# Kernel tuning notes

Hardware: AMD Instinct MI355X
Metric: run time of the kernel (lower is better)

## Reference

```python
import jax, jax.numpy as jnp
import numpy as np

B, N, F_IN = 32, 1024, 64   # batch, num_nodes, diffusion_size[0]
K = 3                        # expansion_step
H = 2                        # num_heads
HID, RAW, OUT, CLS = 128, 128, 128, 2
D1, D2 = 128, 128            # diffusion_size[1], diffusion_size[2]
CAT = D1 + RAW               # concat dim fed to attention (h || h_prime) = 256


def setup_inputs() -> dict:
    key = jax.random.key(0)
    ks = jax.random.split(key, 40)
    g = lambda i, shape: jax.random.normal(ks[i], shape, dtype=jnp.float32) * 0.05
    inp = {
        'X': jax.random.normal(ks[0], (B, N, F_IN), dtype=jnp.float32),
        'A': jax.random.uniform(ks[1], (B, N, N), dtype=jnp.float32),
        # transition tensors / mixing weights (only the 2 layers used in forward)
        'T': g(2, (2, K, N, N)),
        'theta': jnp.full((2, K), 1.0 / K, dtype=jnp.float32),
        # raw feature projection
        'W_raw': g(3, (F_IN, RAW)), 'b_raw': jnp.zeros((RAW,), jnp.float32),
        # diffusion layer linears
        'Wd0': g(4, (F_IN, D1)), 'bd0': jnp.zeros((D1,), jnp.float32),
        'Wd1': g(5, (D1, D2)),   'bd1': jnp.zeros((D2,), jnp.float32),
        # final classifier
        'W_fin': g(6, (OUT, CLS)), 'b_fin': jnp.zeros((CLS,), jnp.float32),
    }
    # two CatMultiAttn blocks: q/k/v projections (CAT->HID), out proj (HID->OUT)
    i = 7
    for l in range(2):
        for nm in ('q', 'k', 'v'):
            inp[f'W{nm}{l}'] = g(i, (CAT, HID)); i += 1
            inp[f'b{nm}{l}'] = jnp.zeros((HID,), jnp.float32)
        inp[f'Wo{l}'] = g(i, (HID, OUT)); i += 1
        inp[f'bo{l}'] = jnp.zeros((OUT,), jnp.float32)
    return inp


def _diffusion(theta_l, T_l, h, A, W, b):
    # Q = sum_k theta_k * T_k  (generalized graph diffusion transition)
    Q = jnp.einsum('k,kij->ij', theta_l, T_l)          # [N,N]
    S = Q[None, :, :] * A                               # [B,N,N] mask by adjacency
    z = jnp.einsum('bij,bjf->bif', S, h)                # diffuse features
    return jax.nn.relu(z @ W + b)


def _cat_attn(h, hp, Wq, bq, Wk, bk, Wv, bv, Wo, bo):
    # concatenate diffused + embedding features, multi-head self-attn over nodes
    x = jnp.concatenate([h, hp], axis=-1)               # [B,N,CAT]
    b, n, _ = x.shape
    q = (x @ Wq + bq).reshape(b, n, H, HID // H)
    k = (x @ Wk + bk).reshape(b, n, H, HID // H)
    v = (x @ Wv + bv).reshape(b, n, H, HID // H)
    scale = jnp.asarray(1.0 / np.sqrt(HID // H), x.dtype)
    s = jnp.einsum('bnhd,bmhd->bhnm', q, k) * scale     # [B,H,N,N]
    p = jax.nn.softmax(s, axis=-1)
    ctx = jnp.einsum('bhnm,bmhd->bnhd', p, v).reshape(b, n, HID)
    return jax.nn.relu(ctx @ Wo + bo)


def reference(X, A, T, theta, W_raw, b_raw, Wd0, bd0, Wd1, bd1,
              W_fin, b_fin,
              Wq0, bq0, Wk0, bk0, Wv0, bv0, Wo0, bo0,
              Wq1, bq1, Wk1, bk1, Wv1, bv1, Wo1, bo1):
    theta_soft = jax.nn.softmax(theta, axis=-1)         # [2,K]
    h_prime = X @ W_raw + b_raw                          # [B,N,RAW]
    # layer 0
    h = _diffusion(theta_soft[0], T[0], X, A, Wd0, bd0)  # [B,N,D1]
    h_prime = _cat_attn(h, h_prime, Wq0, bq0, Wk0, bk0, Wv0, bv0, Wo0, bo0)
    # layer 1 (residual fusion)
    h = _diffusion(theta_soft[1], T[1], h, A, Wd1, bd1)  # [B,N,D2]
    h_prime = h_prime + _cat_attn(h, h_prime, Wq1, bq1, Wk1, bk1, Wv1, bv1, Wo1, bo1)
    return h_prime @ W_fin + b_fin                       # [B,N,CLS]
```

## Files before the change

kernel.cpp:

```cpp
#include <hip/hip_runtime.h>
#include <hip/hip_bf16.h>

typedef __hip_bfloat16 bf16;
typedef __attribute__((ext_vector_type(8))) short s8b;
typedef __attribute__((ext_vector_type(4))) short s4b;
typedef __attribute__((ext_vector_type(4))) float f4;

#define BB   32
#define NN   1024
#define FIN  64
#define HEADS 2
#define DH   64
#define HIDD 128
#define SZQ  ((size_t)BB * NN * HIDD)

__device__ __forceinline__ ushort f2bf(float x) {
    bf16 h = __float2bfloat16(x);
    return *(ushort*)&h;
}
__device__ __forceinline__ float bfbits2f(ushort h) {
    union { uint u; float f; } c; c.u = (uint)h << 16; return c.f;
}
__device__ __forceinline__ uint pk_bf16(float lo, float hi) {
    return (uint)f2bf(lo) | ((uint)f2bf(hi) << 16);
}
union U8 { short s[8]; s8b v; };
union U4 { short s[4]; s4b v; };
union UQ { ushort u[8]; s8b v; };

__global__ __launch_bounds__(256) void setup_kernel(
        const float* __restrict__ raw, const float* __restrict__ d0,
        const float* __restrict__ d1,
        const float* __restrict__ q0w, const float* __restrict__ k0w,
        const float* __restrict__ v0w, const float* __restrict__ o0w,
        const float* __restrict__ q1w, const float* __restrict__ k1w,
        const float* __restrict__ v1w, const float* __restrict__ o1w,
        ushort* __restrict__ Whi, ushort* __restrict__ Wlo,
        const float* __restrict__ T, const float* __restrict__ theta,
        ushort* __restrict__ Q0hi, ushort* __restrict__ Q0lo,
        ushort* __restrict__ Q1hi, ushort* __restrict__ Q1lo,
        const float* __restrict__ X,
        ushort* __restrict__ XT_hi, ushort* __restrict__ XT_lo) {
    __shared__ float tile[64][65];
    const int bid = blockIdx.x;
    const int t = threadIdx.x;
    if (bid < 1024) {
        int id = bid * 256 + t;
        const float* src; int K, off;
        if      (id <   8192) { src = raw; K =  64; off = 0; }
        else if (id <  16384) { src = d0;  K =  64; off = 8192; }
        else if (id <  32768) { src = d1;  K = 128; off = 16384; }
        else if (id <  65536) { src = q0w; K = 256; off = 32768; }
        else if (id <  98304) { src = k0w; K = 256; off = 65536; }
        else if (id < 131072) { src = v0w; K = 256; off = 98304; }
        else if (id < 147456) { src = o0w; K = 128; off = 131072; }
        else if (id < 180224) { src = q1w; K = 256; off = 147456; }
        else if (id < 212992) { src = k1w; K = 256; off = 180224; }
        else if (id < 245760) { src = v1w; K = 256; off = 212992; }
        else                  { src = o1w; K = 128; off = 245760; }
        int il = id - off;
        int k = il >> 7, c = il & 127;
        float w = src[il];
        ushort h = f2bf(w);
        Whi[off + c * K + k] = h;
        Wlo[off + c * K + k] = f2bf(w - bfbits2f(h));
    } else if (bid < 1536) {
        const int tb = bid - 1024;
        const int b  = tb >> 4;
        const int n0 = (tb & 15) * 64;
        {
            int nl = t >> 2, f0 = (t & 3) * 16;
            const float* xp = X + ((size_t)b * NN + n0 + nl) * 64 + f0;
#pragma unroll
            for (int i = 0; i < 16; i += 4)
                *(float4*)&tile[nl][f0 + i] = *(const float4*)(xp + i);
        }
        __syncthreads();
        {
            int f = t >> 2, n1 = (t & 3) * 16;
            U8 h0, h1, l0, l1;
#pragma unroll
            for (int i = 0; i < 16; i++) {
                float v = tile[n1 + i][f];
                ushort hh = f2bf(v);
                ushort ll = f2bf(v - bfbits2f(hh));
                if (i < 8) { h0.s[i] = (short)hh; l0.s[i] = (short)ll; }
                else       { h1.s[i - 8] = (short)hh; l1.s[i - 8] = (short)ll; }
            }
            size_t gb = ((size_t)b * 64 + f) * NN + n0 + n1;
            *(s8b*)&XT_hi[gb]     = h0.v;  *(s8b*)&XT_hi[gb + 8] = h1.v;
            *(s8b*)&XT_lo[gb]     = l0.v;  *(s8b*)&XT_lo[gb + 8] = l1.v;
        }
    } else {
        const int layer = (bid < 2048) ? 0 : 1;
        ushort* Qhi = layer ? Q1hi : Q0hi;
        ushort* Qlo = layer ? Q1lo : Q0lo;
        float t0 = theta[layer * 3 + 0];
        float t1 = theta[layer * 3 + 1];
        float t2 = theta[layer * 3 + 2];
        float m  = fmaxf(t0, fmaxf(t1, t2));
        float e0 = expf(t0 - m), e1 = expf(t1 - m), e2 = expf(t2 - m);
        float inv = 1.0f / (e0 + e1 + e2);
        e0 *= inv; e1 *= inv; e2 *= inv;
        size_t base = ((size_t)((bid - 1536) & 511) * 256 + t) * 8;
        const float* Tl = T + (size_t)layer * 3 * NN * NN;
        U8 hi, lo;
#pragma unroll
        for (int i = 0; i < 8; i++) {
            float q = e0 * Tl[base + i]
                    + e1 * Tl[base + i + (size_t)NN * NN]
                    + e2 * Tl[base + i + (size_t)2 * NN * NN];
            ushort hh = f2bf(q);
            hi.s[i] = (short)hh;
            lo.s[i] = (short)f2bf(q - bfbits2f(hh));
        }
        *(s8b*)&Qhi[base] = hi.v;
        *(s8b*)&Qlo[base] = lo.v;
    }
}

template<int F>
__global__ __launch_bounds__(512, 4) void diffusion_mfma_kernel(
        const ushort* __restrict__ Qhi, const ushort* __restrict__ Qlo,
        const float* __restrict__ A,
        const ushort* __restrict__ hT_hi, const ushort* __restrict__ hT_lo,
        float* __restrict__ z) {
    constexpr int SS  = 72;
    constexpr int NT  = F / 16;
    constexpr int NCW = NT / 4;
    __shared__ short Shi[64][SS], Slo[64][SS];
    __shared__ short Hhi[F][SS],  Hlo[F][SS];

    const int bidx = blockIdx.x;
    const int u  = bidx >> 3;
    const int b  = (bidx & 7) + 8 * (u >> 4);
    const int i0 = (u & 15) * 64;
    const int t  = threadIdx.x;
    const int w  = t >> 6, lane = t & 63;
    const int quad = lane >> 4, c = lane & 15;
    const int rh = w >> 2;
    const int ch = w & 3;

    const int srow = t >> 3, scol = (t & 7) * 8;
    const float*  Ap = A   + ((size_t)b * NN + i0 + srow) * NN + scol;
    const ushort* Qh = Qhi + (size_t)(i0 + srow) * NN + scol;
    const ushort* Ql = Qlo + (size_t)(i0 + srow) * NN + scol;
    constexpr int HTR = 512 / F;
    constexpr int HJ  = 64 / HTR;
    constexpr int HV  = HJ / 8;
    const int hrow = t / HTR, hcol = (t % HTR) * HJ;
    const ushort* Hh = hT_hi + ((size_t)b * F + hrow) * NN + hcol;
    const ushort* Hl = hT_lo + ((size_t)b * F + hrow) * NN + hcol;

    f4 acc[2][NCW];
#pragma unroll
    for (int st = 0; st < 2; st++)
#pragma unroll
        for (int i = 0; i < NCW; i++) acc[st][i] = (f4){0.f, 0.f, 0.f, 0.f};

    float4 a0 = *(const float4*)Ap, a1 = *(const float4*)(Ap + 4);
    s8b hhv[HV], hlv[HV];
#pragma unroll
    for (int vv = 0; vv < HV; vv++) {
        hhv[vv] = *(const s8b*)(Hh + 8 * vv);
        hlv[vv] = *(const s8b*)(Hl + 8 * vv);
    }

#pragma unroll 1
    for (int j0 = 0; j0 < NN; j0 += 64) {
        UQ qh, ql;
        qh.v = *(const s8b*)(Qh + j0);
        ql.v = *(const s8b*)(Ql + j0);
        __syncthreads();
        {
            float av[8] = {a0.x, a0.y, a0.z, a0.w, a1.x, a1.y, a1.z, a1.w};
            U8 hi, lo;
#pragma unroll
            for (int i = 0; i < 8; i++) {
                float q = bfbits2f(qh.u[i]) + bfbits2f(ql.u[i]);
                float s = q * av[i];
                ushort hb = f2bf(s);
                hi.s[i] = (short)hb;
                lo.s[i] = (short)f2bf(s - bfbits2f(hb));
            }
            *(s8b*)&Shi[srow][scol] = hi.v;
            *(s8b*)&Slo[srow][scol] = lo.v;
#pragma unroll
            for (int vv = 0; vv < HV; vv++) {
                *(s8b*)&Hhi[hrow][hcol + 8 * vv] = hhv[vv];
                *(s8b*)&Hlo[hrow][hcol + 8 * vv] = hlv[vv];
            }
        }
        if (j0 + 64 < NN) {
            a0 = *(const float4*)(Ap + j0 + 64);
            a1 = *(const float4*)(Ap + j0 + 68);
#pragma unroll
            for (int vv = 0; vv < HV; vv++) {
                hhv[vv] = *(const s8b*)(Hh + j0 + 64 + 8 * vv);
                hlv[vv] = *(const s8b*)(Hl + j0 + 64 + 8 * vv);
            }
        }
        __syncthreads();

#pragma unroll
        for (int ks = 0; ks < 2; ks++) {
            s8b ah0 = *(const s8b*)&Shi[32 * rh + c][ks * 32 + quad * 8];
            s8b al0 = *(const s8b*)&Slo[32 * rh + c][ks * 32 + quad * 8];
            s8b ah1 = *(const s8b*)&Shi[32 * rh + 16 + c][ks * 32 + quad * 8];
            s8b al1 = *(const s8b*)&Slo[32 * rh + 16 + c][ks * 32 + quad * 8];
#pragma unroll
            for (int ctn = 0; ctn < NCW; ctn++) {
                const int nt = ch * NCW + ctn;
                s8b bhi = *(const s8b*)&Hhi[nt * 16 + c][ks * 32 + quad * 8];
                s8b blo = *(const s8b*)&Hlo[nt * 16 + c][ks * 32 + quad * 8];
                acc[0][ctn] = __builtin_amdgcn_mfma_f32_16x16x32_bf16(ah0, bhi, acc[0][ctn], 0, 0, 0);
                acc[0][ctn] = __builtin_amdgcn_mfma_f32_16x16x32_bf16(al0, bhi, acc[0][ctn], 0, 0, 0);
                acc[0][ctn] = __builtin_amdgcn_mfma_f32_16x16x32_bf16(ah0, blo, acc[0][ctn], 0, 0, 0);
                acc[1][ctn] = __builtin_amdgcn_mfma_f32_16x16x32_bf16(ah1, bhi, acc[1][ctn], 0, 0, 0);
                acc[1][ctn] = __builtin_amdgcn_mfma_f32_16x16x32_bf16(al1, bhi, acc[1][ctn], 0, 0, 0);
                acc[1][ctn] = __builtin_amdgcn_mfma_f32_16x16x32_bf16(ah1, blo, acc[1][ctn], 0, 0, 0);
            }
        }
    }
#pragma unroll
    for (int st = 0; st < 2; st++)
#pragma unroll
        for (int ctn = 0; ctn < NCW; ctn++)
#pragma unroll
            for (int r = 0; r < 4; r++)
                z[((size_t)b * NN + i0 + 32 * rh + 16 * st + quad * 4 + r) * F
                  + (ch * NCW + ctn) * 16 + c] = acc[st][ctn][r];
}

template<int K1, int K2, int CB, bool RELU, bool RESID, int OMODE>
__global__ __launch_bounds__(256) void dense_mfma_kernel(
        const float* __restrict__ in1, const float* __restrict__ in2,
        const ushort* __restrict__ WT_hi, const ushort* __restrict__ WT_lo,
        const float* __restrict__ bias, const float* __restrict__ biask,
        const float* __restrict__ biasv,
        float* __restrict__ out, ushort* __restrict__ outq,
        ushort* __restrict__ hiT, ushort* __restrict__ loT,
        const float* __restrict__ Wfin, const float* __restrict__ bfin,
        float* __restrict__ fout) {
    constexpr int KD  = K1 + K2;
    constexpr int NKT = KD / 32;
    constexpr int NCH = CB / 32;
    __shared__ short Xhi[64][40], Xlo[64][40];
    __shared__ short Whi[CB][40], Wlo[CB][40];
    __shared__ float red[64][2];

    const int r0 = blockIdx.x * 64;
    const int c0 = blockIdx.y * CB;
    const int t  = threadIdx.x;
    const int w  = t >> 6, lane = t & 63;
    const int quad = lane >> 4, c = lane & 15;
    const int rh = w >> 1;
    const int ch = w & 1;

    f4 acc[2][NCH];
#pragma unroll
    for (int st = 0; st < 2; st++)
#pragma unroll
        for (int i = 0; i < NCH; i++) acc[st][i] = (f4){0.f, 0.f, 0.f, 0.f};

    for (int kt = 0; kt < NKT; kt++) {
        const int k0 = kt * 32;
        __syncthreads();
        {
            int row = t >> 2, kk = (t & 3) * 8;
            int g = r0 + row;
            const float* p;
            if (K2 > 0) {
                int k = k0 + kk;
                p = (k < K1) ? (in1 + (size_t)g * K1 + k)
                             : (in2 + (size_t)g * K2 + (k - K1));
            } else {
                p = in1 + (size_t)g * K1 + k0 + kk;
            }
            float4 a = *(const float4*)p, bq = *(const float4*)(p + 4);
            float sv[8] = {a.x, a.y, a.z, a.w, bq.x, bq.y, bq.z, bq.w};
            U8 hi, lo;
#pragma unroll
            for (int i = 0; i < 8; i++) {
                ushort hh = f2bf(sv[i]);
                hi.s[i] = (short)hh;
                lo.s[i] = (short)f2bf(sv[i] - bfbits2f(hh));
            }
            *(s8b*)&Xhi[row][kk] = hi.v;
            *(s8b*)&Xlo[row][kk] = lo.v;
        }
        {
#pragma unroll
            for (int p = 0; p < CB / 64; p++) {
                int cc = p * 64 + (t >> 2), kk = (t & 3) * 8;
                size_t gsrc = (size_t)(c0 + cc) * KD + k0 + kk;
                *(s8b*)&Whi[cc][kk] = *(const s8b*)&WT_hi[gsrc];
                *(s8b*)&Wlo[cc][kk] = *(const s8b*)&WT_lo[gsrc];
            }
        }
        __syncthreads();

        s8b ah0 = *(const s8b*)&Xhi[32 * rh + c][quad * 8];
        s8b al0 = *(const s8b*)&Xlo[32 * rh + c][quad * 8];
        s8b ah1 = *(const s8b*)&Xhi[32 * rh + 16 + c][quad * 8];
        s8b al1 = *(const s8b*)&Xlo[32 * rh + 16 + c][quad * 8];
#pragma unroll
        for (int ct = 0; ct < NCH; ct++) {
            s8b bh = *(const s8b*)&Whi[ch * (CB / 2) + ct * 16 + c][quad * 8];
            s8b bl = *(const s8b*)&Wlo[ch * (CB / 2) + ct * 16 + c][quad * 8];
            acc[0][ct] = __builtin_amdgcn_mfma_f32_16x16x32_bf16(ah0, bh, acc[0][ct], 0, 0, 0);
            acc[0][ct] = __builtin_amdgcn_mfma_f32_16x16x32_bf16(al0, bh, acc[0][ct], 0, 0, 0);
            acc[0][ct] = __builtin_amdgcn_mfma_f32_16x16x32_bf16(ah0, bl, acc[0][ct], 0, 0, 0);
            acc[1][ct] = __builtin_amdgcn_mfma_f32_16x16x32_bf16(ah1, bh, acc[1][ct], 0, 0, 0);
            acc[1][ct] = __builtin_amdgcn_mfma_f32_16x16x32_bf16(al1, bh, acc[1][ct], 0, 0, 0);
            acc[1][ct] = __builtin_amdgcn_mfma_f32_16x16x32_bf16(ah1, bl, acc[1][ct], 0, 0, 0);
        }
    }

    if (OMODE == 3) {
        float fc[2][2][4];
#pragma unroll
        for (int st = 0; st < 2; st++)
#pragma unroll
            for (int o = 0; o < 2; o++)
#pragma unroll
                for (int r = 0; r < 4; r++) fc[st][o][r] = 0.f;
#pragma unroll
        for (int ct = 0; ct < NCH; ct++) {
            const int col = c0 + ch * (CB / 2) + ct * 16 + c;
            float bv = bias[col];
            float w0 = Wfin[col * 2], w1 = Wfin[col * 2 + 1];
#pragma unroll
            for (int st = 0; st < 2; st++) {
                const int rg = r0 + 32 * rh + 16 * st + quad * 4;
#pragma unroll
                for (int r = 0; r < 4; r++) {
                    float v = acc[st][ct][r] + bv;
                    if (RELU) v = fmaxf(v, 0.f);
                    if (RESID) v += out[(size_t)(rg + r) * 128 + col];
                    fc[st][0][r] += v * w0;
                    fc[st][1][r] += v * w1;
                }
            }
        }
#pragma unroll
        for (int st = 0; st < 2; st++)
#pragma unroll
            for (int r = 0; r < 4; r++) {
                float a0 = fc[st][0][r], a1 = fc[st][1][r];
#pragma unroll
                for (int off = 1; off < 16; off <<= 1) {
                    a0 += __shfl_xor(a0, off, 16);
                    a1 += __shfl_xor(a1, off, 16);
                }
                fc[st][0][r] = a0; fc[st][1][r] = a1;
            }
        if (ch == 1 && c == 0) {
#pragma unroll
            for (int st = 0; st < 2; st++)
#pragma unroll
                for (int r = 0; r < 4; r++) {
                    int lr = 32 * rh + 16 * st + quad * 4 + r;
                    red[lr][0] = fc[st][0][r];
                    red[lr][1] = fc[st][1][r];
                }
        }
        __syncthreads();
        if (ch == 0 && c == 0) {
#pragma unroll
            for (int st = 0; st < 2; st++)
#pragma unroll
                for (int r = 0; r < 4; r++) {
                    int lr = 32 * rh + 16 * st + quad * 4 + r;
                    size_t row = (size_t)r0 + lr;
                    fout[row * 2]     = fc[st][0][r] + red[lr][0] + bfin[0];
                    fout[row * 2 + 1] = fc[st][1][r] + red[lr][1] + bfin[1];
                }
        }
        return;
    }
#pragma unroll
    for (int st = 0; st < 2; st++) {
        const int row_g0 = r0 + 32 * rh + 16 * st + quad * 4;
#pragma unroll
        for (int ct = 0; ct < NCH; ct++) {
            const int col = c0 + ch * (CB / 2) + ct * 16 + c;
            if (OMODE == 1) {
                int tensor = col >> 7, cc2 = col & 127;
                float bv = (tensor == 0 ? bias : tensor == 1 ? biask : biasv)[cc2];
                int head = cc2 >> 6, d = cc2 & 63;
                int b = row_g0 >> 10, n = row_g0 & 1023;
                if (tensor == 2) {
                    U4 pk;
#pragma unroll
                    for (int r = 0; r < 4; r++) pk.s[r] = (short)f2bf(acc[st][ct][r] + bv);
                    size_t addr = (((size_t)b * HEADS + head) * 64 + d) * NN + n;
                    *(s4b*)&outq[2 * SZQ + addr] = pk.v;
                } else {
                    ushort* dst = outq + (size_t)tensor * SZQ
                                + (((size_t)b * HEADS + head) * NN + n) * 64 + d;
#pragma unroll
                    for (int r = 0; r < 4; r++) dst[(size_t)r * 64] = f2bf(acc[st][ct][r] + bv);
                }
            } else {
                float bv = bias[col];
                float vv[4];
#pragma unroll
                for (int r = 0; r < 4; r++) {
                    float v = acc[st][ct][r] + bv;
                    if (RELU) v = fmaxf(v, 0.f);
                    size_t o = (size_t)(row_g0 + r) * 128 + col;
                    if (RESID) v += out[o];
                    out[o] = v;
                    vv[r] = v;
                }
                if (OMODE == 2) {
                    int b = row_g0 >> 10, n = row_g0 & 1023;
                    U4 ph, pl;
#pragma unroll
                    for (int r = 0; r < 4; r++) {
                        ushort hh = f2bf(vv[r]);
                        ph.s[r] = (short)hh;
                        pl.s[r] = (short)f2bf(vv[r] - bfbits2f(hh));
                    }
                    size_t tb = ((size_t)b * 128 + col) * NN + n;
                    *(s4b*)&hiT[tb] = ph.v;
                    *(s4b*)&loT[tb] = pl.v;
                }
            }
        }
    }
}

__global__ __launch_bounds__(256) void attn_mfma_kernel(const ushort* __restrict__ q,
                                                        const ushort* __restrict__ k,
                                                        const ushort* __restrict__ vt,
                                                        float* __restrict__ ctx) {
    __shared__ short Ks[128][72];
    __shared__ short Vt[64][136];

    const int bidx = blockIdx.x;
    const int u  = bidx >> 3;
    const int bh = (bidx & 7) + 8 * (u >> 4);
    const int n0 = (u & 15) * 64;
    const int b  = bh >> 1, h = bh & 1;
    const int t  = threadIdx.x;
    const int w  = t >> 6;
    const int lane = t & 63;
    const int quad = lane >> 4, c = lane & 15;
    const size_t kvbase = (size_t)bh * NN * 64;
    const float scale = 0.125f;

    s8b qf0, qf1;
    {
        const ushort* qrow = q + kvbase + (size_t)(n0 + 16 * w + c) * 64;
        qf0 = *(const s8b*)(qrow + quad * 8);
        qf1 = *(const s8b*)(qrow + 32 + quad * 8);
    }

    f4 O[4];
#pragma unroll
    for (int i = 0; i < 4; i++) O[i] = (f4){0.f, 0.f, 0.f, 0.f};
    float l_i = 0.f;

    for (int kt0 = 0; kt0 < NN; kt0 += 128) {
        __syncthreads();
        {
            int key = t >> 2, d0 = (t & 3) * 16;
#pragma unroll
            for (int half = 0; half < 2; half++) {
                const ushort* kr = k + kvbase + (size_t)(kt0 + 64 * half + key) * 64 + d0;
                *(s8b*)&Ks[64 * half + key][d0]     = *(const s8b*)kr;
                *(s8b*)&Ks[64 * half + key][d0 + 8] = *(const s8b*)(kr + 8);
            }
            int d = t >> 2, ch = (t & 3) * 32;
            const ushort* vr = vt + kvbase + (size_t)d * NN + kt0 + ch;
            *(s8b*)&Vt[d][ch]      = *(const s8b*)vr;
            *(s8b*)&Vt[d][ch + 8]  = *(const s8b*)(vr + 8);
            *(s8b*)&Vt[d][ch + 16] = *(const s8b*)(vr + 16);
            *(s8b*)&Vt[d][ch + 24] = *(const s8b*)(vr + 24);
        }
        __syncthreads();

        f4 sg[4][2];
#pragma unroll
        for (int g = 0; g < 4; g++) {
            const int kb = g * 32;
            sg[g][0] = (f4){0.f, 0.f, 0.f, 0.f};
            sg[g][1] = (f4){0.f, 0.f, 0.f, 0.f};
#pragma unroll
            for (int ch = 0; ch < 2; ch++) {
                s8b ka = *(const s8b*)&Ks[kb + c][ch * 32 + quad * 8];
                s8b kB = *(const s8b*)&Ks[kb + 16 + c][ch * 32 + quad * 8];
                s8b qf = ch ? qf1 : qf0;
                sg[g][0] = __builtin_amdgcn_mfma_f32_16x16x32_bf16(ka, qf, sg[g][0], 0, 0, 0);
                sg[g][1] = __builtin_amdgcn_mfma_f32_16x16x32_bf16(kB, qf, sg[g][1], 0, 0, 0);
            }
        }
        float pv[4][8];
        float ps = 0.f;
#pragma unroll
        for (int g = 0; g < 4; g++)
#pragma unroll
            for (int r = 0; r < 4; r++) {
                pv[g][r]     = __expf(sg[g][0][r] * scale);
                pv[g][4 + r] = __expf(sg[g][1][r] * scale);
                ps += pv[g][r] + pv[g][4 + r];
            }
        ps += __shfl_xor(ps, 16);
        ps += __shfl_xor(ps, 32);
        l_i += ps;

        int addr0 = ((((2 * quad) & 3) << 4) | c) << 2;
        int addr1 = ((((2 * quad + 1) & 3) << 4) | c) << 2;
        int tsel = quad >> 1;
#pragma unroll
        for (int g = 0; g < 4; g++) {
            const int kb = g * 32;
            uint Da01 = pk_bf16(pv[g][0], pv[g][1]), Da23 = pk_bf16(pv[g][2], pv[g][3]);
            uint Db01 = pk_bf16(pv[g][4], pv[g][5]), Db23 = pk_bf16(pv[g][6], pv[g][7]);
            int A01_0 = __builtin_amdgcn_ds_bpermute(addr0, (int)Da01);
            int A23_0 = __builtin_amdgcn_ds_bpermute(addr0, (int)Da23);
            int B01_0 = __builtin_amdgcn_ds_bpermute(addr0, (int)Db01);
            int B23_0 = __builtin_amdgcn_ds_bpermute(addr0, (int)Db23);
            int A01_1 = __builtin_amdgcn_ds_bpermute(addr1, (int)Da01);
            int A23_1 = __builtin_amdgcn_ds_bpermute(addr1, (int)Da23);
            int B01_1 = __builtin_amdgcn_ds_bpermute(addr1, (int)Db01);
            int B23_1 = __builtin_amdgcn_ds_bpermute(addr1, (int)Db23);
            union { int i[4]; s8b s; } pf;
            pf.i[0] = tsel ? B01_0 : A01_0;
            pf.i[1] = tsel ? B23_0 : A23_0;
            pf.i[2] = tsel ? B01_1 : A01_1;
            pf.i[3] = tsel ? B23_1 : A23_1;
#pragma unroll
            for (int dt = 0; dt < 4; dt++) {
                s8b vf = *(const s8b*)&Vt[16 * dt + c][kb + quad * 8];
                O[dt] = __builtin_amdgcn_mfma_f32_16x16x32_bf16(vf, pf.s, O[dt], 0, 0, 0);
            }
        }
    }

    float inv = 1.0f / l_i;
    float* crow = ctx + ((size_t)b * NN + n0 + 16 * w + c) * HIDD + h * DH;
#pragma unroll
    for (int dt = 0; dt < 4; dt++)
#pragma unroll
        for (int r = 0; r < 4; r++)
            crow[16 * dt + 4 * quad + r] = O[dt][r] * inv;
}

extern "C" void kernel_launch(void* const* d_in, const int* in_sizes, int n_in,
                              void* d_out, int out_size, void* d_ws, size_t ws_size,
                              hipStream_t stream) {
    (void)in_sizes; (void)n_in; (void)out_size; (void)ws_size;
    const float* X     = (const float*)d_in[0];
    const float* A     = (const float*)d_in[1];
    const float* T     = (const float*)d_in[2];
    const float* theta = (const float*)d_in[3];
    const float* W_raw = (const float*)d_in[4];
    const float* b_raw = (const float*)d_in[5];
    const float* Wd0   = (const float*)d_in[6];
    const float* bd0   = (const float*)d_in[7];
    const float* Wd1   = (const float*)d_in[8];
    const float* bd1   = (const float*)d_in[9];
    const float* W_fin = (const float*)d_in[10];
    const float* b_fin = (const float*)d_in[11];
    const float* Wq0 = (const float*)d_in[12]; const float* bq0 = (const float*)d_in[13];
    const float* Wk0 = (const float*)d_in[14]; const float* bk0 = (const float*)d_in[15];
    const float* Wv0 = (const float*)d_in[16]; const float* bv0 = (const float*)d_in[17];
    const float* Wo0 = (const float*)d_in[18]; const float* bo0 = (const float*)d_in[19];
    const float* Wq1 = (const float*)d_in[20]; const float* bq1 = (const float*)d_in[21];
    const float* Wk1 = (const float*)d_in[22]; const float* bk1 = (const float*)d_in[23];
    const float* Wv1 = (const float*)d_in[24]; const float* bv1 = (const float*)d_in[25];
    const float* Wo1 = (const float*)d_in[26]; const float* bo1 = (const float*)d_in[27];

    float* ws   = (float*)d_ws;
    const size_t SZ = (size_t)BB * NN * HIDD;
    ushort* Q0hi = (ushort*)ws;
    ushort* Q0lo = Q0hi + (size_t)NN * NN;
    float* hp   = ws + (size_t)NN * NN;
    float* h    = hp + SZ;
    float* z    = h + SZ;
    ushort* qb  = (ushort*)(z + SZ);
    ushort* kb  = qb + SZ;
    ushort* XT_hi = qb + 3 * SZ;
    ushort* XT_lo = XT_hi + SZ / 2;
    ushort* hT_hi = XT_lo + SZ / 2;
    ushort* hT_lo = hT_hi + SZ;
    ushort* WT_hi = hT_lo + SZ;
    ushort* WT_lo = WT_hi + 262144;
    ushort* Q1hi = WT_lo + 262144;
    ushort* Q1lo = Q1hi + (size_t)NN * NN;

    const int OFF_RAW = 0, OFF_D0 = 8192, OFF_D1 = 16384, OFF_QKV0 = 32768,
              OFF_O0 = 131072, OFF_QKV1 = 147456, OFF_O1 = 245760;

    const int attnGrid = BB * HEADS * (NN / 64);
    const int diffGrid = BB * (NN / 64);
    const dim3 dg1(512, 1), dg2(512, 2);

    setup_kernel<<<2560, 256, 0, stream>>>(W_raw, Wd0, Wd1, Wq0, Wk0, Wv0, Wo0,
                                           Wq1, Wk1, Wv1, Wo1, WT_hi, WT_lo,
                                           T, theta, Q0hi, Q0lo, Q1hi, Q1lo,
                                           X, XT_hi, XT_lo);

    dense_mfma_kernel<64, 0, 128, false, false, 0><<<dg1, 256, 0, stream>>>(
        X, nullptr, WT_hi + OFF_RAW, WT_lo + OFF_RAW, b_raw, nullptr, nullptr,
        hp, nullptr, nullptr, nullptr, nullptr, nullptr, nullptr);
    diffusion_mfma_kernel<64><<<diffGrid, 512, 0, stream>>>(Q0hi, Q0lo, A, XT_hi, XT_lo, z);
    dense_mfma_kernel<64, 0, 128, true, false, 2><<<dg1, 256, 0, stream>>>(
        z, nullptr, WT_hi + OFF_D0, WT_lo + OFF_D0, bd0, nullptr, nullptr,
        h, nullptr, hT_hi, hT_lo, nullptr, nullptr, nullptr);
    dense_mfma_kernel<128, 128, 192, false, false, 1><<<dg2, 256, 0, stream>>>(
        h, hp, WT_hi + OFF_QKV0, WT_lo + OFF_QKV0, bq0, bk0, bv0,
        nullptr, qb, nullptr, nullptr, nullptr, nullptr, nullptr);
    attn_mfma_kernel<<<attnGrid, 256, 0, stream>>>(qb, kb, qb + 2 * SZ, z);
    dense_mfma_kernel<128, 0, 128, true, false, 0><<<dg1, 256, 0, stream>>>(
        z, nullptr, WT_hi + OFF_O0, WT_lo + OFF_O0, bo0, nullptr, nullptr,
        hp, nullptr, nullptr, nullptr, nullptr, nullptr, nullptr);

    diffusion_mfma_kernel<128><<<diffGrid, 512, 0, stream>>>(Q1hi, Q1lo, A, hT_hi, hT_lo, z);
    dense_mfma_kernel<128, 0, 128, true, false, 0><<<dg1, 256, 0, stream>>>(
        z, nullptr, WT_hi + OFF_D1, WT_lo + OFF_D1, bd1, nullptr, nullptr,
        h, nullptr, nullptr, nullptr, nullptr, nullptr, nullptr);
    dense_mfma_kernel<128, 128, 192, false, false, 1><<<dg2, 256, 0, stream>>>(
        h, hp, WT_hi + OFF_QKV1, WT_lo + OFF_QKV1, bq1, bk1, bv1,
        nullptr, qb, nullptr, nullptr, nullptr, nullptr, nullptr);
    attn_mfma_kernel<<<attnGrid, 256, 0, stream>>>(qb, kb, qb + 2 * SZ, z);
    dense_mfma_kernel<128, 0, 128, true, true, 3><<<dg1, 256, 0, stream>>>(
        z, nullptr, WT_hi + OFF_O1, WT_lo + OFF_O1, bo1, nullptr, nullptr,
        hp, nullptr, nullptr, nullptr, W_fin, b_fin, (float*)d_out);
}
```

Baseline: 512.6 us.

## Fuse diffusion matmul with following dense projection and remap QKV grid for XCD locality

The diffusion kernel now keeps its 64-row z tile in shared memory as split bf16 hi/lo and directly applies the following linear layer (bias, ReLU, optional transposed hi/lo output). This removes the fp32 z round-trip through global memory and two separate dense launches. The QKV dense launch also becomes a 1-D grid remapped so that blocks sharing rows land on the same XCD. The cost is extra shared-memory reuse and a second MFMA phase inside each diffusion block.

```diff
diff --git a/kernel.cpp b/kernel.cpp
--- a/kernel.cpp
+++ b/kernel.cpp
@@ -119,17 +119,30 @@
     }
 }
 
-template<int F>
-__global__ __launch_bounds__(512, 4) void diffusion_mfma_kernel(
+template<int F, bool WRITE_HT>
+__global__ __launch_bounds__(512, 4) void diff_dense_kernel(
         const ushort* __restrict__ Qhi, const ushort* __restrict__ Qlo,
         const float* __restrict__ A,
         const ushort* __restrict__ hT_hi, const ushort* __restrict__ hT_lo,
-        float* __restrict__ z) {
+        const ushort* __restrict__ WT_hi, const ushort* __restrict__ WT_lo,
+        const float* __restrict__ bias,
+        float* __restrict__ hout,
+        ushort* __restrict__ hiT, ushort* __restrict__ loT) {
     constexpr int SS  = 72;
     constexpr int NT  = F / 16;
     constexpr int NCW = NT / 4;
-    __shared__ short Shi[64][SS], Slo[64][SS];
-    __shared__ short Hhi[F][SS],  Hlo[F][SS];
+    constexpr int SZ2 = F + 8;
+    constexpr int P1 = 2 * 64 * SS + 2 * F * SS;
+    constexpr int P2 = 2 * 64 * SZ2 + 2 * 128 * 40;
+    __shared__ short smem[(P1 > P2) ? P1 : P2];
+    short* Shi = smem;
+    short* Slo = Shi + 64 * SS;
+    short* Hhi = Slo + 64 * SS;
+    short* Hlo = Hhi + (size_t)F * SS;
+    short* Zhi = smem;
+    short* Zlo = Zhi + 64 * SZ2;
+    short* Wsh = Zlo + 64 * SZ2;
+    short* Wsl = Wsh + 128 * 40;
 
     const int bidx = blockIdx.x;
     const int u  = bidx >> 3;
@@ -183,12 +196,12 @@
                 hi.s[i] = (short)hb;
                 lo.s[i] = (short)f2bf(s - bfbits2f(hb));
             }
-            *(s8b*)&Shi[srow][scol] = hi.v;
-            *(s8b*)&Slo[srow][scol] = lo.v;
+            *(s8b*)&Shi[srow * SS + scol] = hi.v;
+            *(s8b*)&Slo[srow * SS + scol] = lo.v;
 #pragma unroll
             for (int vv = 0; vv < HV; vv++) {
-                *(s8b*)&Hhi[hrow][hcol + 8 * vv] = hhv[vv];
-                *(s8b*)&Hlo[hrow][hcol + 8 * vv] = hlv[vv];
+                *(s8b*)&Hhi[hrow * SS + hcol + 8 * vv] = hhv[vv];
+                *(s8b*)&Hlo[hrow * SS + hcol + 8 * vv] = hlv[vv];
             }
         }
         if (j0 + 64 < NN) {
@@ -204,15 +217,15 @@
 
 #pragma unroll
         for (int ks = 0; ks < 2; ks++) {
-            s8b ah0 = *(const s8b*)&Shi[32 * rh + c][ks * 32 + quad * 8];
-            s8b al0 = *(const s8b*)&Slo[32 * rh + c][ks * 32 + quad * 8];
-            s8b ah1 = *(const s8b*)&Shi[32 * rh + 16 + c][ks * 32 + quad * 8];
-            s8b al1 = *(const s8b*)&Slo[32 * rh + 16 + c][ks * 32 + quad * 8];
+            s8b ah0 = *(const s8b*)&Shi[(32 * rh + c) * SS + ks * 32 + quad * 8];
+            s8b al0 = *(const s8b*)&Slo[(32 * rh + c) * SS + ks * 32 + quad * 8];
+            s8b ah1 = *(const s8b*)&Shi[(32 * rh + 16 + c) * SS + ks * 32 + quad * 8];
+            s8b al1 = *(const s8b*)&Slo[(32 * rh + 16 + c) * SS + ks * 32 + quad * 8];
 #pragma unroll
             for (int ctn = 0; ctn < NCW; ctn++) {
                 const int nt = ch * NCW + ctn;
-                s8b bhi = *(const s8b*)&Hhi[nt * 16 + c][ks * 32 + quad * 8];
-                s8b blo = *(const s8b*)&Hlo[nt * 16 + c][ks * 32 + quad * 8];
+                s8b bhi = *(const s8b*)&Hhi[(nt * 16 + c) * SS + ks * 32 + quad * 8];
+                s8b blo = *(const s8b*)&Hlo[(nt * 16 + c) * SS + ks * 32 + quad * 8];
                 acc[0][ctn] = __builtin_amdgcn_mfma_f32_16x16x32_bf16(ah0, bhi, acc[0][ctn], 0, 0, 0);
                 acc[0][ctn] = __builtin_amdgcn_mfma_f32_16x16x32_bf16(al0, bhi, acc[0][ctn], 0, 0, 0);
                 acc[0][ctn] = __builtin_amdgcn_mfma_f32_16x16x32_bf16(ah0, blo, acc[0][ctn], 0, 0, 0);
@@ -222,14 +235,86 @@
             }
         }
     }
+
+    __syncthreads();
 #pragma unroll
     for (int st = 0; st < 2; st++)
 #pragma unroll
         for (int ctn = 0; ctn < NCW; ctn++)
 #pragma unroll
-            for (int r = 0; r < 4; r++)
-                z[((size_t)b * NN + i0 + 32 * rh + 16 * st + quad * 4 + r) * F
-                  + (ch * NCW + ctn) * 16 + c] = acc[st][ctn][r];
+            for (int r = 0; r < 4; r++) {
+                const int row = 32 * rh + 16 * st + quad * 4 + r;
+                const int col = (ch * NCW + ctn) * 16 + c;
+                float v = acc[st][ctn][r];
+                ushort hh = f2bf(v);
+                Zhi[row * SZ2 + col] = (short)hh;
+                Zlo[row * SZ2 + col] = (short)f2bf(v - bfbits2f(hh));
+            }
+
+    const int rh2 = w >> 2;
+    const int ch2 = w & 3;
+    f4 acc2[2][2];
+#pragma unroll
+    for (int st = 0; st < 2; st++)
+#pragma unroll
+        for (int i = 0; i < 2; i++) acc2[st][i] = (f4){0.f, 0.f, 0.f, 0.f};
+
+    constexpr int NKT = F / 32;
+    for (int kt = 0; kt < NKT; kt++) {
+        __syncthreads();
+        {
+            int cc = t >> 2, kk = (t & 3) * 8;
+            size_t gsrc = (size_t)cc * F + kt * 32 + kk;
+            *(s8b*)&Wsh[cc * 40 + kk] = *(const s8b*)&WT_hi[gsrc];
+            *(s8b*)&Wsl[cc * 40 + kk] = *(const s8b*)&WT_lo[gsrc];
+        }
+        __syncthreads();
+
+        s8b ah0 = *(const s8b*)&Zhi[(32 * rh2 + c) * SZ2 + kt * 32 + quad * 8];
+        s8b al0 = *(const s8b*)&Zlo[(32 * rh2 + c) * SZ2 + kt * 32 + quad * 8];
+        s8b ah1 = *(const s8b*)&Zhi[(32 * rh2 + 16 + c) * SZ2 + kt * 32 + quad * 8];
+        s8b al1 = *(const s8b*)&Zlo[(32 * rh2 + 16 + c) * SZ2 + kt * 32 + quad * 8];
+#pragma unroll
+        for (int ct = 0; ct < 2; ct++) {
+            s8b bh = *(const s8b*)&Wsh[(ch2 * 32 + ct * 16 + c) * 40 + quad * 8];
+            s8b bl = *(const s8b*)&Wsl[(ch2 * 32 + ct * 16 + c) * 40 + quad * 8];
+            acc2[0][ct] = __builtin_amdgcn_mfma_f32_16x16x32_bf16(ah0, bh, acc2[0][ct], 0, 0, 0);
+            acc2[0][ct] = __builtin_amdgcn_mfma_f32_16x16x32_bf16(al0, bh, acc2[0][ct], 0, 0, 0);
+            acc2[0][ct] = __builtin_amdgcn_mfma_f32_16x16x32_bf16(ah0, bl, acc2[0][ct], 0, 0, 0);
+            acc2[1][ct] = __builtin_amdgcn_mfma_f32_16x16x32_bf16(ah1, bh, acc2[1][ct], 0, 0, 0);
+            acc2[1][ct] = __builtin_amdgcn_mfma_f32_16x16x32_bf16(al1, bh, acc2[1][ct], 0, 0, 0);
+            acc2[1][ct] = __builtin_amdgcn_mfma_f32_16x16x32_bf16(ah1, bl, acc2[1][ct], 0, 0, 0);
+        }
+    }
+
+#pragma unroll
+    for (int st = 0; st < 2; st++) {
+        const int rg0 = i0 + 32 * rh2 + 16 * st + quad * 4;
+#pragma unroll
+        for (int ct = 0; ct < 2; ct++) {
+            const int col = ch2 * 32 + ct * 16 + c;
+            float bv = bias[col];
+            float vv[4];
+#pragma unroll
+            for (int r = 0; r < 4; r++) {
+                float v = fmaxf(acc2[st][ct][r] + bv, 0.f);
+                hout[((size_t)b * NN + rg0 + r) * 128 + col] = v;
+                vv[r] = v;
+            }
+            if (WRITE_HT) {
+                U4 ph, pl;
+#pragma unroll
+                for (int r = 0; r < 4; r++) {
+                    ushort hh = f2bf(vv[r]);
+                    ph.s[r] = (short)hh;
+                    pl.s[r] = (short)f2bf(vv[r] - bfbits2f(hh));
+                }
+                size_t tb = ((size_t)b * 128 + col) * NN + rg0;
+                *(s4b*)&hiT[tb] = ph.v;
+                *(s4b*)&loT[tb] = pl.v;
+            }
+        }
+    }
 }
 
 template<int K1, int K2, int CB, bool RELU, bool RESID, int OMODE>
@@ -239,7 +324,6 @@
         const float* __restrict__ bias, const float* __restrict__ biask,
         const float* __restrict__ biasv,
         float* __restrict__ out, ushort* __restrict__ outq,
-        ushort* __restrict__ hiT, ushort* __restrict__ loT,
         const float* __restrict__ Wfin, const float* __restrict__ bfin,
         float* __restrict__ fout) {
     constexpr int KD  = K1 + K2;
@@ -249,8 +333,14 @@
     __shared__ short Whi[CB][40], Wlo[CB][40];
     __shared__ float red[64][2];
 
-    const int r0 = blockIdx.x * 64;
-    const int c0 = blockIdx.y * CB;
+    int bx, by;
+    if (OMODE == 1) {
+        const int xcd = blockIdx.x & 7, qq = blockIdx.x >> 3;
+        by = qq & 1;
+        bx = ((qq >> 1) << 3) | xcd;
+    } else { bx = blockIdx.x; by = blockIdx.y; }
+    const int r0 = bx * 64;
+    const int c0 = by * CB;
     const int t  = threadIdx.x;
     const int w  = t >> 6, lane = t & 63;
     const int quad = lane >> 4, c = lane & 15;
@@ -404,7 +494,6 @@
                 }
             } else {
                 float bv = bias[col];
-                float vv[4];
 #pragma unroll
                 for (int r = 0; r < 4; r++) {
                     float v = acc[st][ct][r] + bv;
@@ -412,20 +501,6 @@
                     size_t o = (size_t)(row_g0 + r) * 128 + col;
                     if (RESID) v += out[o];
                     out[o] = v;
-                    vv[r] = v;
-                }
-                if (OMODE == 2) {
-                    int b = row_g0 >> 10, n = row_g0 & 1023;
-                    U4 ph, pl;
-#pragma unroll
-                    for (int r = 0; r < 4; r++) {
-                        ushort hh = f2bf(vv[r]);
-                        ph.s[r] = (short)hh;
-                        pl.s[r] = (short)f2bf(vv[r] - bfbits2f(hh));
-                    }
-                    size_t tb = ((size_t)b * 128 + col) * NN + n;
-                    *(s4b*)&hiT[tb] = ph.v;
-                    *(s4b*)&loT[tb] = pl.v;
                 }
             }
         }
@@ -597,7 +672,7 @@
 
     const int attnGrid = BB * HEADS * (NN / 64);
     const int diffGrid = BB * (NN / 64);
-    const dim3 dg1(512, 1), dg2(512, 2);
+    const dim3 dg1(512, 1);
 
     setup_kernel<<<2560, 256, 0, stream>>>(W_raw, Wd0, Wd1, Wq0, Wk0, Wv0, Wo0,
                                            Wq1, Wk1, Wv1, Wo1, WT_hi, WT_lo,
@@ -606,28 +681,26 @@
 
     dense_mfma_kernel<64, 0, 128, false, false, 0><<<dg1, 256, 0, stream>>>(
         X, nullptr, WT_hi + OFF_RAW, WT_lo + OFF_RAW, b_raw, nullptr, nullptr,
-        hp, nullptr, nullptr, nullptr, nullptr, nullptr, nullptr);
-    diffusion_mfma_kernel<64><<<diffGrid, 512, 0, stream>>>(Q0hi, Q0lo, A, XT_hi, XT_lo, z);
-    dense_mfma_kernel<64, 0, 128, true, false, 2><<<dg1, 256, 0, stream>>>(
-        z, nullptr, WT_hi + OFF_D0, WT_lo + OFF_D0, bd0, nullptr, nullptr,
-        h, nullptr, hT_hi, hT_lo, nullptr, nullptr, nullptr);
-    dense_mfma_kernel<128, 128, 192, false, false, 1><<<dg2, 256, 0, stream>>>(
+        hp, nullptr, nullptr, nullptr, nullptr);
+    diff_dense_kernel<64, true><<<diffGrid, 512, 0, stream>>>(
+        Q0hi, Q0lo, A, XT_hi, XT_lo, WT_hi + OFF_D0, WT_lo + OFF_D0, bd0,
+        h, hT_hi, hT_lo);
+    dense_mfma_kernel<128, 128, 192, false, false, 1><<<1024, 256, 0, stream>>>(
         h, hp, WT_hi + OFF_QKV0, WT_lo + OFF_QKV0, bq0, bk0, bv0,
-        nullptr, qb, nullptr, nullptr, nullptr, nullptr, nullptr);
+        nullptr, qb, nullptr, nullptr, nullptr);
     attn_mfma_kernel<<<attnGrid, 256, 0, stream>>>(qb, kb, qb + 2 * SZ, z);
     dense_mfma_kernel<128, 0, 128, true, false, 0><<<dg1, 256, 0, stream>>>(
         z, nullptr, WT_hi + OFF_O0, WT_lo + OFF_O0, bo0, nullptr, nullptr,
-        hp, nullptr, nullptr, nullptr, nullptr, nullptr, nullptr);
-
-    diffusion_mfma_kernel<128><<<diffGrid, 512, 0, stream>>>(Q1hi, Q1lo, A, hT_hi, hT_lo, z);
-    dense_mfma_kernel<128, 0, 128, true, false, 0><<<dg1, 256, 0, stream>>>(
-        z, nullptr, WT_hi + OFF_D1, WT_lo + OFF_D1, bd1, nullptr, nullptr,
-        h, nullptr, nullptr, nullptr, nullptr, nullptr, nullptr);
-    dense_mfma_kernel<128, 128, 192, false, false, 1><<<dg2, 256, 0, stream>>>(
+        hp, nullptr, nullptr, nullptr, nullptr);
+
+    diff_dense_kernel<128, false><<<diffGrid, 512, 0, stream>>>(
+        Q1hi, Q1lo, A, hT_hi, hT_lo, WT_hi + OFF_D1, WT_lo + OFF_D1, bd1,
+        h, nullptr, nullptr);
+    dense_mfma_kernel<128, 128, 192, false, false, 1><<<1024, 256, 0, stream>>>(
         h, hp, WT_hi + OFF_QKV1, WT_lo + OFF_QKV1, bq1, bk1, bv1,
-        nullptr, qb, nullptr, nullptr, nullptr, nullptr, nullptr);
+        nullptr, qb, nullptr, nullptr, nullptr);
     attn_mfma_kernel<<<attnGrid, 256, 0, stream>>>(qb, kb, qb + 2 * SZ, z);
     dense_mfma_kernel<128, 0, 128, true, true, 3><<<dg1, 256, 0, stream>>>(
         z, nullptr, WT_hi + OFF_O1, WT_lo + OFF_O1, bo1, nullptr, nullptr,
-        hp, nullptr, nullptr, nullptr, W_fin, b_fin, (float*)d_out);
+        hp, nullptr, W_fin, b_fin, (float*)d_out);
 }
```

New measurement: 505.6 us. Within noise of the previous version (-1.4%).
